# Performance work log

Hardware: AMD Instinct MI355X
Metric: run time of the kernel (lower is better)

Reference implementation:

```python
import jax, jax.numpy as jnp
import numpy as np

# CTC-CRF constants (bonito defaults): state_len=5, alphabet='NACGT' -> n_base=4
STATE_LEN = 5
N_BASE = 4
S = N_BASE ** STATE_LEN          # 1024 states
NZ = N_BASE + 1                  # 5 incoming transitions per state (stay + 4 moves)
C = S * NZ                       # 5120 score channels per timestep


def _make_idx():
    # idx[s] = indices into alpha (previous states) feeding state s.
    # Matches torch: cat([arange(S)[:,None], arange(S).repeat_interleave(n_base).reshape(n_base,-1).T], 1)
    a = np.arange(S)
    idx = np.concatenate([a[:, None], np.repeat(a, N_BASE).reshape(N_BASE, S).T], axis=1)
    return jnp.asarray(idx, dtype=jnp.int32)  # [S, NZ]


def setup_inputs() -> dict:
    key = jax.random.key(0)
    T, N = 2000, 32
    scores = jax.random.normal(key, (T, N, C), dtype=jnp.float32)
    return {"scores": scores}


def reference(scores) -> jnp.ndarray:
    # Faithful jax version of CTC_CRF.logZ(scores) with the Log semiring:
    #   alpha[t+1] = logsumexp(Ms[t] + alpha[t][:, idx], axis=-1)
    #   logZ = logsumexp(alpha[T] + vT, axis=1)
    T, N, _ = scores.shape
    idx = _make_idx()                      # [S, NZ] int32
    Ms = scores.reshape(T, N, S, NZ)       # [T, N, S, NZ]
    v0 = jnp.zeros((N, S), dtype=scores.dtype)  # semiring one = 0.0
    vT = jnp.zeros((N, S), dtype=scores.dtype)

    def step(alpha, Ms_t):
        # alpha: [N, S]; gather predecessors -> [N, S, NZ]; semiring mul = add; sum = logsumexp
        a_next = jax.nn.logsumexp(Ms_t + alpha[:, idx], axis=-1)
        return a_next, None

    alpha_T, _ = jax.lax.scan(step, v0, Ms)
    return jax.nn.logsumexp(alpha_T + vT, axis=1)  # [N]
```

## Files before the change

kernel.cpp:

```cpp
#include <hip/hip_runtime.h>
#include <cstdint>
#include <cstddef>


#define NB 32
#define SD 1024
#define CD 5120

typedef float f4a __attribute__((ext_vector_type(4), aligned(4)));

__device__ __forceinline__ float fexp2(float x) { return __builtin_amdgcn_exp2f(x); }
__device__ __forceinline__ float flog2(float x) { return __builtin_amdgcn_logf(x); }

template <int CTRL>
__device__ __forceinline__ float dppq(float v) {
  return __int_as_float(
      __builtin_amdgcn_update_dpp(0, __float_as_int(v), CTRL, 0xF, 0xF, true));
}

__global__ void __launch_bounds__(1024) ctc_logz(const float* __restrict__ scores,
                                                 float* __restrict__ out, int T) {
  __shared__ float ap[2 * SD];
  __shared__ float red[16];

  const int u = threadIdx.x;
  const int n = blockIdx.x;
  const int lane = u & 63;
  const int wid = u >> 6;
  const int p = u >> 2, c = u & 3;
  const int rdoff = (c << 8) | (p ^ (c << 3));
  const int wroff = u ^ ((u & 0x300) >> 5);

  ap[u] = 1.f; ap[SD + u] = 1.f;
  float a_cur = 1.f;
  float nLf = 0.f;
  int Lnext = 0, cacc = 0;

  const float K = 1.44269504088896340736f;
  const float LN2 = 0.69314718055994530942f;

  const float* sn = scores + (size_t)n * CD + (size_t)u * 5;
  const size_t tstr = (size_t)NB * CD;
  const size_t str4 = 4 * tstr;

  auto CP = [&](int t, const f4a& qa, float qb) {
    const int rb = ((t + 1) & 1) * SD;
    const float vr = ap[rb + rdoff];
    const float R = ap[rb];
    const float p0 = dppq<0x00>(vr);
    const float p1 = dppq<0x55>(vr);
    const float p2 = dppq<0xAA>(vr);
    const float p3 = dppq<0xFF>(vr);
    float e0 = fexp2(__builtin_fmaf(qa.x, K, nLf));
    float e1 = fexp2(__builtin_fmaf(qa.y, K, nLf));
    float e2 = fexp2(__builtin_fmaf(qa.z, K, nLf));
    float e3 = fexp2(__builtin_fmaf(qa.w, K, nLf));
    float e4 = fexp2(__builtin_fmaf(qb,   K, nLf));
    float s = e0 * a_cur;
    s = __builtin_fmaf(e1, p0, s);
    s = __builtin_fmaf(e2, p1, s);
    s = __builtin_fmaf(e3, p2, s);
    s = __builtin_fmaf(e4, p3, s);
    a_cur = s;
    cacc += Lnext;
    ap[(t & 1) * SD + wroff] = s;
    const int xb = ((__float_as_int(R) >> 23) & 0xFF) - 127;
    Lnext = xb >> 2;
    nLf = (float)(-Lnext);
    asm volatile("s_waitcnt lgkmcnt(0)\n\ts_barrier" ::: "memory");
  };

#define PRO(cc)                                                             \
  const float* P##cc = sn + (size_t)((cc) < T ? (cc) : T - 1) * tstr;       \
  f4a qa##cc = *(const f4a*)P##cc;                                          \
  float qb##cc = P##cc[4];                                                  \
  P##cc += str4;
  PRO(0) PRO(1) PRO(2) PRO(3)
#undef PRO

  __syncthreads();

#define RL(cc)                                                              \
  qa##cc = *(const f4a*)P##cc;                                              \
  qb##cc = P##cc[4];                                                        \
  P##cc += str4;

  int t = 0;
  for (; t + 8 <= T; t += 4) {
    CP(t + 0, qa0, qb0); RL(0)
    CP(t + 1, qa1, qb1); RL(1)
    CP(t + 2, qa2, qb2); RL(2)
    CP(t + 3, qa3, qb3); RL(3)
  }
#undef RL

#define EPI1(cc)                                                            \
  if (t + (cc) < T) {                                                       \
    CP(t + (cc), qa##cc, qb##cc);                                           \
    if (t + 4 + (cc) < T) { qa##cc = *(const f4a*)P##cc; qb##cc = P##cc[4]; }\
  }
  EPI1(0) EPI1(1) EPI1(2) EPI1(3)
#undef EPI1
  t += 4;
#define EPI2(cc) if (t + (cc) < T) CP(t + (cc), qa##cc, qb##cc);
  EPI2(0) EPI2(1) EPI2(2) EPI2(3)
#undef EPI2

  float v = a_cur;
#pragma unroll
  for (int d = 1; d < 64; d <<= 1) v += __shfl_xor(v, d, 64);
  if (lane == 0) red[wid] = v;
  __syncthreads();
  if (u == 0) {
    float ssum = red[0];
#pragma unroll
    for (int i = 1; i < 16; ++i) ssum += red[i];
    out[n] = LN2 * ((float)cacc + flog2(ssum));
  }
}

extern "C" void kernel_launch(void* const* d_in, const int* in_sizes, int n_in,
                              void* d_out, int out_size, void* d_ws, size_t ws_size,
                              hipStream_t stream) {
  const float* scores = (const float*)d_in[0];
  float* out = (float*)d_out;
  const long long tot = (long long)in_sizes[0];
  const int T = (int)(tot / ((long long)NB * CD));
  ctc_logz<<<dim3(NB), dim3(1024), 0, stream>>>(scores, out, T);
}
```

Before: 761.3 us.

## Add helper prefetch blocks that warm cache ahead of the sequential recursion

Launches 224 extra helper blocks alongside the 32 recursion blocks. The helpers read upcoming timesteps of the score tensor a bounded distance ahead of each batch's progress counter, which the main blocks publish through relaxed atomics every 8 steps. The goal is to pull the scores into L2/MALL so the latency-bound recurrence sees cache hits instead of HBM misses. The cost is an extra init kernel, spin-waiting helper blocks that compete for bandwidth and CUs, and a dependence on co-residency and cache capacity.

```diff
diff --git a/kernel.cpp b/kernel.cpp
--- a/kernel.cpp
+++ b/kernel.cpp
@@ -6,6 +6,8 @@
 #define NB 32
 #define SD 1024
 #define CD 5120
+#define AHEAD 24
+#define DONE_S 0x7fffffff
 
 typedef float f4a __attribute__((ext_vector_type(4), aligned(4)));
 
@@ -18,13 +20,48 @@
       __builtin_amdgcn_update_dpp(0, __float_as_int(v), CTRL, 0xF, 0xF, true));
 }
 
+__global__ void init_prog(int* prog) {
+  if (threadIdx.x < NB) prog[threadIdx.x] = 0;
+}
+
 __global__ void __launch_bounds__(1024) ctc_logz(const float* __restrict__ scores,
-                                                 float* __restrict__ out, int T) {
+                                                 float* __restrict__ out,
+                                                 int* __restrict__ prog, int T) {
+  const int bid = blockIdx.x;
+
+  if (bid >= NB) {
+    const int pb = bid - NB;
+    const int n = pb & 31;
+    const int k = pb >> 5;
+    const int wid = threadIdx.x >> 6;
+    const int lane = threadIdx.x & 63;
+    const int q = k * 16 + wid;
+    const float* sb = scores + (size_t)n * CD + (size_t)lane * 4;
+    const size_t tstr = (size_t)NB * CD;
+    float acc = 0.f;
+    for (int t = q; t < T; t += 112) {
+      int p = __hip_atomic_load(&prog[n], __ATOMIC_RELAXED, __HIP_MEMORY_SCOPE_AGENT);
+      while (p != DONE_S && p + AHEAD <= t) {
+        __builtin_amdgcn_s_sleep(32);
+        p = __hip_atomic_load(&prog[n], __ATOMIC_RELAXED, __HIP_MEMORY_SCOPE_AGENT);
+      }
+      if (p == DONE_S) break;
+      const float* s = sb + (size_t)t * tstr;
+#pragma unroll
+      for (int i = 0; i < 20; ++i) {
+        f4a v = *(const f4a*)(s + i * 256);
+        acc += v.x + v.y + v.z + v.w;
+      }
+    }
+    asm volatile("" ::"v"(acc));
+    return;
+  }
+
   __shared__ float ap[2 * SD];
   __shared__ float red[16];
 
   const int u = threadIdx.x;
-  const int n = blockIdx.x;
+  const int n = bid;
   const int lane = u & 63;
   const int wid = u >> 6;
   const int p = u >> 2, c = u & 3;
@@ -67,6 +104,8 @@
     const int xb = ((__float_as_int(R) >> 23) & 0xFF) - 127;
     Lnext = xb >> 2;
     nLf = (float)(-Lnext);
+    if (((t & 7) == 0) && (u == 0))
+      __hip_atomic_store(&prog[n], t, __ATOMIC_RELAXED, __HIP_MEMORY_SCOPE_AGENT);
     asm volatile("s_waitcnt lgkmcnt(0)\n\ts_barrier" ::: "memory");
   };
 
@@ -106,6 +145,9 @@
   EPI2(0) EPI2(1) EPI2(2) EPI2(3)
 #undef EPI2
 
+  if (u == 0)
+    __hip_atomic_store(&prog[n], DONE_S, __ATOMIC_RELAXED, __HIP_MEMORY_SCOPE_AGENT);
+
   float v = a_cur;
 #pragma unroll
   for (int d = 1; d < 64; d <<= 1) v += __shfl_xor(v, d, 64);
@@ -124,7 +166,9 @@
                               hipStream_t stream) {
   const float* scores = (const float*)d_in[0];
   float* out = (float*)d_out;
+  int* prog = (int*)d_ws;
   const long long tot = (long long)in_sizes[0];
   const int T = (int)(tot / ((long long)NB * CD));
-  ctc_logz<<<dim3(NB), dim3(1024), 0, stream>>>(scores, out, T);
+  init_prog<<<dim3(1), dim3(64), 0, stream>>>(prog);
+  ctc_logz<<<dim3(256), dim3(1024), 0, stream>>>(scores, out, prog, T);
 }
```

Measured after the change: 1.220 ms. 1.6x slower.
